# Optimization experiments

Measured on AMD Instinct MI355X. Metric: run time of the kernel, lower is better.

## Reference

```python
import jax, jax.numpy as jnp
import numpy as np

BN_EPS = 1e-5

def conv1x1(x_bcn, w, b):
    # x: [B,C,N], w: [O,C], b: [O] -> [B,O,N]
    return jnp.einsum('oc,bcn->bon', w, x_bcn) + b[None, :, None]

def bn_eval(x, g, b):
    # inference BN with running_mean=0, running_var=1
    return x / jnp.sqrt(1.0 + BN_EPS) * g + b

def setup_inputs() -> dict:
    key = jax.random.key(0)
    ks = jax.random.split(key, 24)
    B, C, H, W = 2, 256, 64, 64
    Cq = C // 4
    s = lambda k, sh, fan: jax.random.normal(k, sh, jnp.float32) * (1.0 / np.sqrt(fan))
    inp = {
        'input1': jax.random.normal(ks[0], (B, C, H, W), jnp.float32),
        'input2': jax.random.normal(ks[1], (B, C, H, W), jnp.float32),
        'q1_w': s(ks[2], (Cq, C), C), 'q1_b': jnp.zeros((Cq,), jnp.float32),
        'k1_w': s(ks[3], (Cq, C), C), 'k1_b': jnp.zeros((Cq,), jnp.float32),
        'v1_w': s(ks[4], (C, C), C),  'v1_b': jnp.zeros((C,), jnp.float32),
        'q2_w': s(ks[5], (Cq, C), C), 'q2_b': jnp.zeros((Cq,), jnp.float32),
        'k2_w': s(ks[6], (Cq, C), C), 'k2_b': jnp.zeros((Cq,), jnp.float32),
        'v2_w': s(ks[7], (C, C), C),  'v2_b': jnp.zeros((C,), jnp.float32),
        'g1_w': s(ks[8], (C, 2 * C), 2 * C), 'g1_b': jnp.zeros((C,), jnp.float32),
        'bn1_g': jnp.ones((C,), jnp.float32), 'bn1_b': jnp.zeros((C,), jnp.float32),
        'g2_w': s(ks[9], (Cq, C), C), 'g2_b': jnp.zeros((Cq,), jnp.float32),
        'bn2_g': jnp.ones((Cq,), jnp.float32), 'bn2_b': jnp.zeros((Cq,), jnp.float32),
        'gamma': jnp.zeros((1,), jnp.float32) + 0.5,  # nonzero so attention branch matters
    }
    return inp

def _attshare(input1, input2, q1_w, q1_b, k1_w, k1_b, v1_w, v1_b,
              q2_w, q2_b, k2_w, k2_b, v2_w, v2_b,
              g1_w, g1_b, bn1_g, bn1_b, g2_w, g2_b, bn2_g, bn2_b, gamma):
    B, C, H, W = input1.shape
    N = H * W
    x1 = input1.reshape(B, C, N)
    x2 = input2.reshape(B, C, N)
    # global attention branch: adaptive avg pool -> conv -> BN -> relu -> conv -> BN -> sigmoid
    pooled = jnp.concatenate([x1, x2], axis=1).mean(axis=2)          # [B, 2C]
    y = jnp.einsum('oc,bc->bo', g1_w, pooled) + g1_b
    y = jax.nn.relu(bn_eval(y, bn1_g, bn1_b))
    y = jnp.einsum('oc,bc->bo', g2_w, y) + g2_b
    g = jax.nn.sigmoid(bn_eval(y, bn2_g, bn2_b))                      # [B, C/4]

    def stream(x, inp4d, qw, qb, kw, kb, vw, vb):
        q = conv1x1(x, qw, qb).transpose(0, 2, 1)   # [B, N, C/4]
        k = conv1x1(x, kw, kb)                       # [B, C/4, N]
        v = conv1x1(x, vw, vb)                       # [B, C, N]
        # bmm(q, g.repeat(N)) has identical columns -> per-row bias
        bias = jnp.einsum('bnc,bc->bn', q, g)        # [B, N]
        attn = jnp.einsum('bnc,bcm->bnm', q, k) + bias[:, :, None]
        attn = jax.nn.softmax(attn, axis=-1)         # [B, N, N]
        out = jnp.einsum('bcj,bij->bci', v, attn)    # [B, C, N]
        return gamma * out.reshape(inp4d.shape) + inp4d

    out1 = stream(x1, input1, q1_w, q1_b, k1_w, k1_b, v1_w, v1_b)
    out2 = stream(x2, input2, q2_w, q2_b, k2_w, k2_b, v2_w, v2_b)
    return out1, out2

def reference(input1, input2, q1_w, q1_b, k1_w, k1_b, v1_w, v1_b,
              q2_w, q2_b, k2_w, k2_b, v2_w, v2_b,
              g1_w, g1_b, bn1_g, bn1_b, g2_w, g2_b, bn2_g, bn2_b, gamma):
    return _attshare(input1, input2, q1_w, q1_b, k1_w, k1_b, v1_w, v1_b,
                     q2_w, q2_b, k2_w, k2_b, v2_w, v2_b,
                     g1_w, g1_b, bn1_g, bn1_b, g2_w, g2_b, bn2_g, bn2_b, gamma)
```

## Files before the change

### kernel.cpp

```cpp
#include <hip/hip_runtime.h>
#include <math.h>

constexpr int B_  = 2;
constexpr int C_  = 256;
constexpr int CQ_ = 64;
constexpr int N_  = 4096;

typedef __attribute__((ext_vector_type(8))) short     short8;
typedef __attribute__((ext_vector_type(8))) _Float16  half8;
typedef __attribute__((ext_vector_type(4))) float     f32x4;

constexpr float SHIFT = 24.0f;

static __device__ __forceinline__ unsigned short f2bf(float x) {
    union { float f; unsigned u; } v; v.f = x;
    unsigned r = (v.u + 0x7FFFu + ((v.u >> 16) & 1u)) >> 16;
    return (unsigned short)r;
}

__global__ __launch_bounds__(256)
void wconv_kernel(const float* __restrict__ q1w, const float* __restrict__ k1w,
                  const float* __restrict__ v1w, const float* __restrict__ q2w,
                  const float* __restrict__ k2w, const float* __restrict__ v2w,
                  _Float16* __restrict__ wb)
{
    int i = (blockIdx.x * 256 + threadIdx.x) * 4;
    const float* src;
    int off;
    if      (i < 16384)  { src = q1w; off = 0; }
    else if (i < 32768)  { src = k1w; off = 16384; }
    else if (i < 98304)  { src = v1w; off = 32768; }
    else if (i < 114688) { src = q2w; off = 98304; }
    else if (i < 131072) { src = k2w; off = 114688; }
    else                 { src = v2w; off = 131072; }
    float4 f = *(const float4*)(src + (i - off));
    _Float16 h0 = (_Float16)f.x, h1 = (_Float16)f.y;
    _Float16 h2 = (_Float16)f.z, h3 = (_Float16)f.w;
    ushort4 u;
    u.x = *(unsigned short*)&h0; u.y = *(unsigned short*)&h1;
    u.z = *(unsigned short*)&h2; u.w = *(unsigned short*)&h3;
    *(ushort4*)((unsigned short*)wb + i) = u;
}

__global__ __launch_bounds__(512)
void proj_kernel(const float* __restrict__ in1, const float* __restrict__ in2,
                 const _Float16* __restrict__ wb,
                 const float* __restrict__ q1b, const float* __restrict__ k1b,
                 const float* __restrict__ v1b, const float* __restrict__ q2b,
                 const float* __restrict__ k2b, const float* __restrict__ v2b,
                 _Float16* __restrict__ q_ws, _Float16* __restrict__ kf_ws,
                 unsigned short* __restrict__ vf_ws)
{
    __shared__ _Float16 Xs[64 * 264];
    const int bs = blockIdx.y, s = bs >> 1, bb = bs & 1;
    const int n0 = blockIdx.x * 64;
    const float* x = (s ? in2 : in1) + (size_t)bb * C_ * N_;
    const int tid = threadIdx.x;
    const int lane = tid & 63, wave = tid >> 6, quad = lane >> 4, l15 = lane & 15;

    #pragma unroll
    for (int rep = 0; rep < 8; ++rep) {
        int idx = rep * 512 + tid;
        int c = idx >> 4, ng = idx & 15;
        float4 f = *(const float4*)(x + (size_t)c * N_ + n0 + ng * 4);
        Xs[(ng * 4 + 0) * 264 + c] = (_Float16)f.x;
        Xs[(ng * 4 + 1) * 264 + c] = (_Float16)f.y;
        Xs[(ng * 4 + 2) * 264 + c] = (_Float16)f.z;
        Xs[(ng * 4 + 3) * 264 + c] = (_Float16)f.w;
    }
    __syncthreads();

    const _Float16* wqs = wb + (size_t)s * 98304;
    const _Float16* wks = wqs + 16384;
    const _Float16* wvs = wks + 16384;

    {
        const int m = wave >> 2, nb = wave & 3;
        const _Float16* W = m ? wks : wqs;
        const float* bias = m ? (s ? k2b : k1b) : (s ? q2b : q1b);
        half8 af[8];
        #pragma unroll
        for (int kh = 0; kh < 8; ++kh)
            af[kh] = *(const half8*)(&Xs[(16 * nb + l15) * 264 + quad * 8 + kh * 32]);
        f32x4 a4[4];
        #pragma unroll
        for (int o = 0; o < 4; ++o) a4[o] = (f32x4){0.f, 0.f, 0.f, 0.f};
        #pragma unroll
        for (int kh = 0; kh < 8; ++kh)
            #pragma unroll
            for (int o = 0; o < 4; ++o) {
                half8 bf = *(const half8*)(W + (size_t)(16 * o + l15) * C_ + quad * 8 + kh * 32);
                a4[o] = __builtin_amdgcn_mfma_f32_16x16x32_f16(af[kh], bf, a4[o], 0, 0, 0);
            }
        if (m == 0) {
            _Float16* outp = q_ws + (size_t)bs * N_ * CQ_;
            #pragma unroll
            for (int o = 0; o < 4; ++o) {
                float bv = bias[16 * o + l15];
                #pragma unroll
                for (int r = 0; r < 4; ++r) {
                    int n = n0 + 16 * nb + quad * 4 + r;
                    outp[(size_t)n * CQ_ + 16 * o + l15] = (_Float16)(a4[o][r] + bv);
                }
            }
        } else {
            unsigned short* kd = (unsigned short*)(kf_ws) + (size_t)bs * 262144;
            const int jt = (n0 >> 4) + nb;
            const int e = l15 & 7;
            #pragma unroll
            for (int o = 0; o < 4; ++o) {
                float bv = bias[16 * o + l15];
                const int kh = o >> 1;
                const int lhi = ((o & 1) * 2 + (l15 >> 3)) * 16;
                #pragma unroll
                for (int r = 0; r < 4; ++r) {
                    _Float16 hv = (_Float16)(a4[o][r] + bv);
                    int lane_f = lhi + quad * 4 + r;
                    kd[(size_t)(jt * 2 + kh) * 512 + lane_f * 8 + e] = *(unsigned short*)&hv;
                }
            }
        }
    }

    {
        const float* vb = s ? v2b : v1b;
        unsigned short* vd = vf_ws + (size_t)bs * 1048576;
        f32x4 v4[2][4];
        #pragma unroll
        for (int o = 0; o < 2; ++o)
            #pragma unroll
            for (int nt = 0; nt < 4; ++nt) v4[o][nt] = (f32x4){0.f, 0.f, 0.f, 0.f};
        #pragma unroll
        for (int kh = 0; kh < 8; ++kh) {
            half8 bf[4], af[2];
            #pragma unroll
            for (int nt = 0; nt < 4; ++nt)
                bf[nt] = *(const half8*)(&Xs[(16 * nt + l15) * 264 + quad * 8 + kh * 32]);
            #pragma unroll
            for (int o = 0; o < 2; ++o)
                af[o] = *(const half8*)(wvs + (size_t)(32 * wave + 16 * o + l15) * C_ + quad * 8 + kh * 32);
            #pragma unroll
            for (int o = 0; o < 2; ++o)
                #pragma unroll
                for (int nt = 0; nt < 4; ++nt)
                    v4[o][nt] = __builtin_amdgcn_mfma_f32_16x16x32_f16(af[o], bf[nt], v4[o][nt], 0, 0, 0);
        }
        const int e = l15 & 7;
        #pragma unroll
        for (int o = 0; o < 2; ++o) {
            const int ct = 2 * wave + o;
            #pragma unroll
            for (int r = 0; r < 4; ++r) {
                int c = 32 * wave + 16 * o + quad * 4 + r;
                float bv = vb[c];
                #pragma unroll
                for (int nt = 0; nt < 4; ++nt) {
                    const int j32 = (n0 >> 5) + (nt >> 1);
                    const int lane_f = ((nt & 1) * 2 + (l15 >> 3)) * 16 + quad * 4 + r;
                    vd[(size_t)(j32 * 16 + ct) * 512 + lane_f * 8 + e] =
                        f2bf(v4[o][nt][r] + bv);
                }
            }
        }
    }
}

__global__ __launch_bounds__(1024)
void flash_kernel(const _Float16* __restrict__ qg,
                  const _Float16* __restrict__ kfg,
                  const unsigned short* __restrict__ vfg,
                  const float* __restrict__ in1, const float* __restrict__ in2,
                  const float* __restrict__ gamma_p, float* __restrict__ out)
{
    __shared__ unsigned short Pt[2][64 * 64];
    __shared__ float lsum[64 * 4];

    const int tid  = threadIdx.x;
    const int lane = tid & 63;
    const int wave = tid >> 6;
    const int quad = lane >> 4;
    const int l15  = lane & 15;
    const int bs   = blockIdx.x & 3;
    const int q0   = (blockIdx.x >> 2) * 64;
    const int s = bs >> 1, bb = bs & 1;
    const int jsub  = wave & 3;
    const int ihalf = (wave >> 2) & 1;
    const int wc = wave & 7;
    const int jh = wave >> 3;

    const _Float16* qp = qg + (size_t)bs * N_ * CQ_;
    const _Float16* kB = kfg + (size_t)bs * 262144 + lane * 8;
    const unsigned short* vB = vfg + (size_t)bs * 1048576 + (size_t)lane * 8;

    unsigned char* ptb0 = (unsigned char*)&Pt[0][0];
    unsigned char* ptb1 = (unsigned char*)&Pt[1][0];

    half8 qf[2][2];
    float lacc[2] = {0.f, 0.f};
    half8 kf[2];
    short8 vf[2];
    f32x4 acc[4][2];
    #pragma unroll
    for (int a = 0; a < 4; ++a)
        #pragma unroll
        for (int bq = 0; bq < 2; ++bq) acc[a][bq] = (f32x4){0.f, 0.f, 0.f, 0.f};

    if (wave < 8) {
        #pragma unroll
        for (int isub = 0; isub < 2; ++isub)
            #pragma unroll
            for (int kh = 0; kh < 2; ++kh)
                qf[isub][kh] = *(const half8*)(
                    qp + (size_t)(q0 + 32 * ihalf + 16 * isub + l15) * CQ_ + quad * 8 + kh * 32);
        kf[0] = *(const half8*)(kB + (size_t)(jsub * 2 + 0) * 512);
        kf[1] = *(const half8*)(kB + (size_t)(jsub * 2 + 1) * 512);
        f32x4 sacc[2];
        sacc[0] = (f32x4){0.f, 0.f, 0.f, 0.f};
        sacc[1] = (f32x4){0.f, 0.f, 0.f, 0.f};
        #pragma unroll
        for (int kh = 0; kh < 2; ++kh)
            #pragma unroll
            for (int isub = 0; isub < 2; ++isub)
                sacc[isub] = __builtin_amdgcn_mfma_f32_16x16x32_f16(
                    kf[kh], qf[isub][kh], sacc[isub], 0, 0, 0);
        #pragma unroll
        for (int isub = 0; isub < 2; ++isub) {
            f32x4 p;
            p.x = __expf(sacc[isub].x - SHIFT);
            p.y = __expf(sacc[isub].y - SHIFT);
            p.z = __expf(sacc[isub].z - SHIFT);
            p.w = __expf(sacc[isub].w - SHIFT);
            lacc[isub] += p.x + p.y + p.z + p.w;
            unsigned pk0, pk1;
            asm("v_cvt_pk_bf16_f32 %0, %1, %2" : "=v"(pk0) : "v"(p.x), "v"(p.y));
            asm("v_cvt_pk_bf16_f32 %0, %1, %2" : "=v"(pk1) : "v"(p.z), "v"(p.w));
            int row = 32 * ihalf + 16 * isub + l15;
            int cb  = (32 * jsub + 8 * quad) ^ ((row & 7) << 4);
            uint2 pbv; pbv.x = pk0; pbv.y = pk1;
            *(uint2*)(ptb0 + row * 128 + cb) = pbv;
        }
        kf[0] = *(const half8*)(kB + (size_t)((4 + jsub) * 2 + 0) * 512);
        kf[1] = *(const half8*)(kB + (size_t)((4 + jsub) * 2 + 1) * 512);
    }
    vf[0] = *(const short8*)(vB + (size_t)(jh * 16 + 2 * wc + 0) * 512);
    vf[1] = *(const short8*)(vB + (size_t)(jh * 16 + 2 * wc + 1) * 512);

    for (int t = 0; t < 64; ++t) {
        unsigned char* ptr = (t & 1) ? ptb1 : ptb0;
        unsigned char* ptw = (t & 1) ? ptb0 : ptb1;

        asm volatile("s_waitcnt lgkmcnt(0)" ::: "memory");
        __builtin_amdgcn_sched_barrier(0);
        __builtin_amdgcn_s_barrier();
        __builtin_amdgcn_sched_barrier(0);

        short8 ap[4];
        #pragma unroll
        for (int is2 = 0; is2 < 4; ++is2) {
            int row = 16 * is2 + l15;
            int cb  = (jh * 64 + quad * 16) ^ ((row & 7) << 4);
            ap[is2] = *(const short8*)(ptr + row * 128 + cb);
        }
        __builtin_amdgcn_s_setprio(1);
        #pragma unroll
        for (int is2 = 0; is2 < 4; ++is2)
            #pragma unroll
            for (int csub = 0; csub < 2; ++csub)
                acc[is2][csub] = __builtin_amdgcn_mfma_f32_16x16x32_bf16(
                    ap[is2], vf[csub], acc[is2][csub], 0, 0, 0);
        __builtin_amdgcn_s_setprio(0);

        if (t < 63) {
            if (wave < 8) {
                f32x4 sacc[2];
                sacc[0] = (f32x4){0.f, 0.f, 0.f, 0.f};
                sacc[1] = (f32x4){0.f, 0.f, 0.f, 0.f};
                #pragma unroll
                for (int kh = 0; kh < 2; ++kh)
                    #pragma unroll
                    for (int isub = 0; isub < 2; ++isub)
                        sacc[isub] = __builtin_amdgcn_mfma_f32_16x16x32_f16(
                            kf[kh], qf[isub][kh], sacc[isub], 0, 0, 0);
                #pragma unroll
                for (int isub = 0; isub < 2; ++isub) {
                    f32x4 p;
                    p.x = __expf(sacc[isub].x - SHIFT);
                    p.y = __expf(sacc[isub].y - SHIFT);
                    p.z = __expf(sacc[isub].z - SHIFT);
                    p.w = __expf(sacc[isub].w - SHIFT);
                    lacc[isub] += p.x + p.y + p.z + p.w;
                    unsigned pk0, pk1;
                    asm("v_cvt_pk_bf16_f32 %0, %1, %2" : "=v"(pk0) : "v"(p.x), "v"(p.y));
                    asm("v_cvt_pk_bf16_f32 %0, %1, %2" : "=v"(pk1) : "v"(p.z), "v"(p.w));
                    int row = 32 * ihalf + 16 * isub + l15;
                    int cb  = (32 * jsub + 8 * quad) ^ ((row & 7) << 4);
                    uint2 pbv; pbv.x = pk0; pbv.y = pk1;
                    *(uint2*)(ptw + row * 128 + cb) = pbv;
                }
                int tk = (t + 2) & 63;
                kf[0] = *(const half8*)(kB + (size_t)((tk * 4 + jsub) * 2 + 0) * 512);
                kf[1] = *(const half8*)(kB + (size_t)((tk * 4 + jsub) * 2 + 1) * 512);
            }
            vf[0] = *(const short8*)(vB + (size_t)((2 * (t + 1) + jh) * 16 + 2 * wc + 0) * 512);
            vf[1] = *(const short8*)(vB + (size_t)((2 * (t + 1) + jh) * 16 + 2 * wc + 1) * 512);
        }
    }

    if (wave < 8) {
        #pragma unroll
        for (int isub = 0; isub < 2; ++isub) {
            float t = lacc[isub];
            t += __shfl_xor(t, 16);
            t += __shfl_xor(t, 32);
            if (quad == 0)
                lsum[(32 * ihalf + 16 * isub + l15) * 4 + jsub] = t;
        }
    }
    __syncthreads();

    float* red = (float*)&Pt[0][0];
    #pragma unroll
    for (int r = 0; r < 4; ++r) {
        if (wave >= 8) {
            *(f32x4*)(red + (size_t)(wave - 8) * 512 + lane * 8 + 0) = acc[r][0];
            *(f32x4*)(red + (size_t)(wave - 8) * 512 + lane * 8 + 4) = acc[r][1];
        }
        __syncthreads();
        if (wave < 8) {
            f32x4 a0 = *(const f32x4*)(red + (size_t)wave * 512 + lane * 8 + 0);
            f32x4 a1 = *(const f32x4*)(red + (size_t)wave * 512 + lane * 8 + 4);
            acc[r][0] += a0;
            acc[r][1] += a1;
        }
        __syncthreads();
    }

    if (wave < 8) {
        const float gamma = gamma_p[0];
        const float* inp = (s ? in2 : in1) + (size_t)bb * C_ * N_;
        float* op = out + (size_t)bs * C_ * N_;
        #pragma unroll
        for (int is2 = 0; is2 < 4; ++is2) {
            float inv[4];
            #pragma unroll
            for (int r = 0; r < 4; ++r) {
                f32x4 t = *(const f32x4*)(&lsum[(16 * is2 + quad * 4 + r) * 4]);
                inv[r] = 1.0f / (t.x + t.y + t.z + t.w);
            }
            #pragma unroll
            for (int csub = 0; csub < 2; ++csub) {
                int c = 32 * wc + 16 * csub + l15;
                #pragma unroll
                for (int r = 0; r < 4; ++r) {
                    int i = q0 + 16 * is2 + quad * 4 + r;
                    size_t idx = (size_t)c * N_ + i;
                    op[idx] = gamma * acc[is2][csub][r] * inv[r] + inp[idx];
                }
            }
        }
    }
}

extern "C" void kernel_launch(void* const* d_in, const int* in_sizes, int n_in,
                              void* d_out, int out_size, void* d_ws, size_t ws_size,
                              hipStream_t stream)
{
    const float* in1 = (const float*)d_in[0];
    const float* in2 = (const float*)d_in[1];
    const float* q1w = (const float*)d_in[2];
    const float* q1b = (const float*)d_in[3];
    const float* k1w = (const float*)d_in[4];
    const float* k1b = (const float*)d_in[5];
    const float* v1w = (const float*)d_in[6];
    const float* v1b = (const float*)d_in[7];
    const float* q2w = (const float*)d_in[8];
    const float* q2b = (const float*)d_in[9];
    const float* k2w = (const float*)d_in[10];
    const float* k2b = (const float*)d_in[11];
    const float* v2w = (const float*)d_in[12];
    const float* v2b = (const float*)d_in[13];
    const float* gamma = (const float*)d_in[22];
    float* out = (float*)d_out;

    _Float16* wb   = (_Float16*)d_ws;
    _Float16* q_ws = wb + 196608;
    _Float16* kf_ws = q_ws + (size_t)4 * N_ * CQ_;
    unsigned short* vf_ws = (unsigned short*)(kf_ws + (size_t)4 * 262144);

    wconv_kernel<<<dim3(192), 256, 0, stream>>>(q1w, k1w, v1w, q2w, k2w, v2w, wb);
    proj_kernel<<<dim3(64, 4), 512, 0, stream>>>(
        in1, in2, wb, q1b, k1b, v1b, q2b, k2b, v2b, q_ws, kf_ws, vf_ws);
    flash_kernel<<<dim3(256), 1024, 0, stream>>>(
        q_ws, kf_ws, vf_ws, in1, in2, gamma, out);
}
```

Measured before the change: 178.2 us.

## Retile PV MFMA per wave to 2x4 and interleave QK softmax

Result: slower. 191.0 us (+7.2%).

```diff
diff --git a/kernel.cpp b/kernel.cpp
--- a/kernel.cpp
+++ b/kernel.cpp
@@ -185,8 +185,9 @@
     const int s = bs >> 1, bb = bs & 1;
     const int jsub  = wave & 3;
     const int ihalf = (wave >> 2) & 1;
-    const int wc = wave & 7;
-    const int jh = wave >> 3;
+    const int wc2 = wave & 3;
+    const int ihh = (wave >> 2) & 1;
+    const int jh  = wave >> 3;
 
     const _Float16* qp = qg + (size_t)bs * N_ * CQ_;
     const _Float16* kB = kfg + (size_t)bs * 262144 + lane * 8;
@@ -198,12 +199,12 @@
     half8 qf[2][2];
     float lacc[2] = {0.f, 0.f};
     half8 kf[2];
-    short8 vf[2];
-    f32x4 acc[4][2];
+    short8 vf[4];
+    f32x4 acc[2][4];
     #pragma unroll
-    for (int a = 0; a < 4; ++a)
-        #pragma unroll
-        for (int bq = 0; bq < 2; ++bq) acc[a][bq] = (f32x4){0.f, 0.f, 0.f, 0.f};
+    for (int a = 0; a < 2; ++a)
+        #pragma unroll
+        for (int bq = 0; bq < 4; ++bq) acc[a][bq] = (f32x4){0.f, 0.f, 0.f, 0.f};
 
     if (wave < 8) {
         #pragma unroll
@@ -242,8 +243,9 @@
         kf[0] = *(const half8*)(kB + (size_t)((4 + jsub) * 2 + 0) * 512);
         kf[1] = *(const half8*)(kB + (size_t)((4 + jsub) * 2 + 1) * 512);
     }
-    vf[0] = *(const short8*)(vB + (size_t)(jh * 16 + 2 * wc + 0) * 512);
-    vf[1] = *(const short8*)(vB + (size_t)(jh * 16 + 2 * wc + 1) * 512);
+    #pragma unroll
+    for (int csub = 0; csub < 4; ++csub)
+        vf[csub] = *(const short8*)(vB + (size_t)(jh * 16 + 4 * wc2 + csub) * 512);
 
     for (int t = 0; t < 64; ++t) {
         unsigned char* ptr = (t & 1) ? ptb1 : ptb0;
@@ -254,55 +256,73 @@
         __builtin_amdgcn_s_barrier();
         __builtin_amdgcn_sched_barrier(0);
 
-        short8 ap[4];
-        #pragma unroll
-        for (int is2 = 0; is2 < 4; ++is2) {
-            int row = 16 * is2 + l15;
-            int cb  = (jh * 64 + quad * 16) ^ ((row & 7) << 4);
-            ap[is2] = *(const short8*)(ptr + row * 128 + cb);
-        }
-        __builtin_amdgcn_s_setprio(1);
-        #pragma unroll
-        for (int is2 = 0; is2 < 4; ++is2)
-            #pragma unroll
-            for (int csub = 0; csub < 2; ++csub)
-                acc[is2][csub] = __builtin_amdgcn_mfma_f32_16x16x32_bf16(
-                    ap[is2], vf[csub], acc[is2][csub], 0, 0, 0);
-        __builtin_amdgcn_s_setprio(0);
+        if (wave < 8 && t < 63) {
+            f32x4 sacc[2];
+            sacc[0] = (f32x4){0.f, 0.f, 0.f, 0.f};
+            sacc[1] = (f32x4){0.f, 0.f, 0.f, 0.f};
+            #pragma unroll
+            for (int kh = 0; kh < 2; ++kh)
+                #pragma unroll
+                for (int isub = 0; isub < 2; ++isub)
+                    sacc[isub] = __builtin_amdgcn_mfma_f32_16x16x32_f16(
+                        kf[kh], qf[isub][kh], sacc[isub], 0, 0, 0);
+            short8 ap[2];
+            #pragma unroll
+            for (int is2l = 0; is2l < 2; ++is2l) {
+                int row = 32 * ihh + 16 * is2l + l15;
+                int cb  = (jh * 64 + quad * 16) ^ ((row & 7) << 4);
+                ap[is2l] = *(const short8*)(ptr + row * 128 + cb);
+            }
+            __builtin_amdgcn_s_setprio(1);
+            #pragma unroll
+            for (int is2l = 0; is2l < 2; ++is2l)
+                #pragma unroll
+                for (int csub = 0; csub < 4; ++csub)
+                    acc[is2l][csub] = __builtin_amdgcn_mfma_f32_16x16x32_bf16(
+                        ap[is2l], vf[csub], acc[is2l][csub], 0, 0, 0);
+            __builtin_amdgcn_s_setprio(0);
+            #pragma unroll
+            for (int isub = 0; isub < 2; ++isub) {
+                f32x4 p;
+                p.x = __expf(sacc[isub].x - SHIFT);
+                p.y = __expf(sacc[isub].y - SHIFT);
+                p.z = __expf(sacc[isub].z - SHIFT);
+                p.w = __expf(sacc[isub].w - SHIFT);
+                lacc[isub] += p.x + p.y + p.z + p.w;
+                unsigned pk0, pk1;
+                asm("v_cvt_pk_bf16_f32 %0, %1, %2" : "=v"(pk0) : "v"(p.x), "v"(p.y));
+                asm("v_cvt_pk_bf16_f32 %0, %1, %2" : "=v"(pk1) : "v"(p.z), "v"(p.w));
+                int row = 32 * ihalf + 16 * isub + l15;
+                int cb  = (32 * jsub + 8 * quad) ^ ((row & 7) << 4);
+                uint2 pbv; pbv.x = pk0; pbv.y = pk1;
+                *(uint2*)(ptw + row * 128 + cb) = pbv;
+            }
+            int tk = (t + 2) & 63;
+            kf[0] = *(const half8*)(kB + (size_t)((tk * 4 + jsub) * 2 + 0) * 512);
+            kf[1] = *(const half8*)(kB + (size_t)((tk * 4 + jsub) * 2 + 1) * 512);
+        } else {
+            short8 ap[2];
+            #pragma unroll
+            for (int is2l = 0; is2l < 2; ++is2l) {
+                int row = 32 * ihh + 16 * is2l + l15;
+                int cb  = (jh * 64 + quad * 16) ^ ((row & 7) << 4);
+                ap[is2l] = *(const short8*)(ptr + row * 128 + cb);
+            }
+            __builtin_amdgcn_s_setprio(1);
+            #pragma unroll
+            for (int is2l = 0; is2l < 2; ++is2l)
+                #pragma unroll
+                for (int csub = 0; csub < 4; ++csub)
+                    acc[is2l][csub] = __builtin_amdgcn_mfma_f32_16x16x32_bf16(
+                        ap[is2l], vf[csub], acc[is2l][csub], 0, 0, 0);
+            __builtin_amdgcn_s_setprio(0);
+        }
 
         if (t < 63) {
-            if (wave < 8) {
-                f32x4 sacc[2];
-                sacc[0] = (f32x4){0.f, 0.f, 0.f, 0.f};
-                sacc[1] = (f32x4){0.f, 0.f, 0.f, 0.f};
-                #pragma unroll
-                for (int kh = 0; kh < 2; ++kh)
-                    #pragma unroll
-                    for (int isub = 0; isub < 2; ++isub)
-                        sacc[isub] = __builtin_amdgcn_mfma_f32_16x16x32_f16(
-                            kf[kh], qf[isub][kh], sacc[isub], 0, 0, 0);
-                #pragma unroll
-                for (int isub = 0; isub < 2; ++isub) {
-                    f32x4 p;
-                    p.x = __expf(sacc[isub].x - SHIFT);
-                    p.y = __expf(sacc[isub].y - SHIFT);
-                    p.z = __expf(sacc[isub].z - SHIFT);
-                    p.w = __expf(sacc[isub].w - SHIFT);
-                    lacc[isub] += p.x + p.y + p.z + p.w;
-                    unsigned pk0, pk1;
-                    asm("v_cvt_pk_bf16_f32 %0, %1, %2" : "=v"(pk0) : "v"(p.x), "v"(p.y));
-                    asm("v_cvt_pk_bf16_f32 %0, %1, %2" : "=v"(pk1) : "v"(p.z), "v"(p.w));
-                    int row = 32 * ihalf + 16 * isub + l15;
-                    int cb  = (32 * jsub + 8 * quad) ^ ((row & 7) << 4);
-                    uint2 pbv; pbv.x = pk0; pbv.y = pk1;
-                    *(uint2*)(ptw + row * 128 + cb) = pbv;
-                }
-                int tk = (t + 2) & 63;
-                kf[0] = *(const half8*)(kB + (size_t)((tk * 4 + jsub) * 2 + 0) * 512);
-                kf[1] = *(const half8*)(kB + (size_t)((tk * 4 + jsub) * 2 + 1) * 512);
-            }
-            vf[0] = *(const short8*)(vB + (size_t)((2 * (t + 1) + jh) * 16 + 2 * wc + 0) * 512);
-            vf[1] = *(const short8*)(vB + (size_t)((2 * (t + 1) + jh) * 16 + 2 * wc + 1) * 512);
+            #pragma unroll
+            for (int csub = 0; csub < 4; ++csub)
+                vf[csub] = *(const short8*)(
+                    vB + (size_t)((2 * (t + 1) + jh) * 16 + 4 * wc2 + csub) * 512);
         }
     }
 
@@ -320,17 +340,18 @@
 
     float* red = (float*)&Pt[0][0];
     #pragma unroll
-    for (int r = 0; r < 4; ++r) {
+    for (int rr = 0; rr < 4; ++rr) {
+        const int a0i = rr >> 1, a0c = (rr & 1) * 2;
         if (wave >= 8) {
-            *(f32x4*)(red + (size_t)(wave - 8) * 512 + lane * 8 + 0) = acc[r][0];
-            *(f32x4*)(red + (size_t)(wave - 8) * 512 + lane * 8 + 4) = acc[r][1];
+            *(f32x4*)(red + (size_t)(wave - 8) * 512 + lane * 8 + 0) = acc[a0i][a0c];
+            *(f32x4*)(red + (size_t)(wave - 8) * 512 + lane * 8 + 4) = acc[a0i][a0c + 1];
         }
         __syncthreads();
         if (wave < 8) {
-            f32x4 a0 = *(const f32x4*)(red + (size_t)wave * 512 + lane * 8 + 0);
-            f32x4 a1 = *(const f32x4*)(red + (size_t)wave * 512 + lane * 8 + 4);
-            acc[r][0] += a0;
-            acc[r][1] += a1;
+            f32x4 b0 = *(const f32x4*)(red + (size_t)wave * 512 + lane * 8 + 0);
+            f32x4 b1 = *(const f32x4*)(red + (size_t)wave * 512 + lane * 8 + 4);
+            acc[a0i][a0c]     += b0;
+            acc[a0i][a0c + 1] += b1;
         }
         __syncthreads();
     }
@@ -340,22 +361,25 @@
         const float* inp = (s ? in2 : in1) + (size_t)bb * C_ * N_;
         float* op = out + (size_t)bs * C_ * N_;
         #pragma unroll
-        for (int is2 = 0; is2 < 4; ++is2) {
+        for (int is2l = 0; is2l < 2; ++is2l) {
             float inv[4];
             #pragma unroll
             for (int r = 0; r < 4; ++r) {
-                f32x4 t = *(const f32x4*)(&lsum[(16 * is2 + quad * 4 + r) * 4]);
+                f32x4 t = *(const f32x4*)(&lsum[(32 * ihh + 16 * is2l + quad * 4 + r) * 4]);
                 inv[r] = 1.0f / (t.x + t.y + t.z + t.w);
             }
-            #pragma unroll
-            for (int csub = 0; csub < 2; ++csub) {
-                int c = 32 * wc + 16 * csub + l15;
-                #pragma unroll
-                for (int r = 0; r < 4; ++r) {
-                    int i = q0 + 16 * is2 + quad * 4 + r;
-                    size_t idx = (size_t)c * N_ + i;
-                    op[idx] = gamma * acc[is2][csub][r] * inv[r] + inp[idx];
-                }
+            const int i0 = q0 + 32 * ihh + 16 * is2l + 4 * quad;
+            #pragma unroll
+            for (int csub = 0; csub < 4; ++csub) {
+                const int c = 64 * wc2 + 16 * csub + l15;
+                const size_t idx = (size_t)c * N_ + i0;
+                float4 r4 = *(const float4*)(inp + idx);
+                float4 o4;
+                o4.x = gamma * acc[is2l][csub][0] * inv[0] + r4.x;
+                o4.y = gamma * acc[is2l][csub][1] * inv[1] + r4.y;
+                o4.z = gamma * acc[is2l][csub][2] * inv[2] + r4.z;
+                o4.w = gamma * acc[is2l][csub][3] * inv[3] + r4.w;
+                *(float4*)(op + idx) = o4;
             }
         }
     }
```
